# Performance work log

Hardware: AMD Instinct MI355X
Metric: run time of the kernel (lower is better)

Reference implementation:

```python
import jax, jax.numpy as jnp
import numpy as np

B, S, HID = 2, 2048, 2560
NH, NKV, HD = 8, 4, 256
Q_SIZE, KV_SIZE = NH * HD, NKV * HD
SCALE = 256.0 ** -0.5
SLIDING_WINDOW = 1024 - 1  # config.sliding_window - 1
ROPE_BASE = 10000.0
EPS = 1e-6


def rmsnorm(x, w, eps=EPS):
    xf = x.astype(jnp.float32)
    out = xf * jax.lax.rsqrt(jnp.mean(xf * xf, axis=-1, keepdims=True) + eps)
    return (out * (1.0 + w.astype(jnp.float32))).astype(x.dtype)


def apply_rope(x, positions):
    # x: [B,S,H,D], neox style (rotate halves)
    d = x.shape[-1]
    inv_freq = 1.0 / (ROPE_BASE ** (jnp.arange(0, d, 2, dtype=jnp.float32) / d))
    freqs = positions.astype(jnp.float32)[..., None] * inv_freq  # [B,S,d/2]
    cos = jnp.cos(freqs)[:, :, None, :]
    sin = jnp.sin(freqs)[:, :, None, :]
    x1, x2 = x[..., : d // 2], x[..., d // 2:]
    return jnp.concatenate([x1 * cos - x2 * sin, x2 * cos + x1 * sin], axis=-1).astype(x.dtype)


def setup_inputs() -> dict:
    key = jax.random.key(0)
    ks = jax.random.split(key, 4)
    positions = jnp.broadcast_to(jnp.arange(S, dtype=jnp.int32)[None, :], (B, S))
    hidden_states = jax.random.normal(ks[0], (B, S, HID), dtype=jnp.float32)
    attention_mask = jnp.ones((B, S), dtype=jnp.int32)
    Wqkv = jax.random.normal(ks[1], (HID, Q_SIZE + 2 * KV_SIZE), dtype=jnp.float32) * (HID ** -0.5)
    Wo = jax.random.normal(ks[2], (Q_SIZE, HID), dtype=jnp.float32) * (Q_SIZE ** -0.5)
    q_norm_w = jnp.zeros((HD,), dtype=jnp.float32)
    k_norm_w = jnp.zeros((HD,), dtype=jnp.float32)
    return {"positions": positions, "hidden_states": hidden_states,
            "attention_mask": attention_mask, "Wqkv": Wqkv, "Wo": Wo,
            "q_norm_w": q_norm_w, "k_norm_w": k_norm_w}


def reference(positions, hidden_states, attention_mask, Wqkv, Wo, q_norm_w, k_norm_w):
    b, s, _ = hidden_states.shape
    qkv = hidden_states @ Wqkv
    q, k, v = jnp.split(qkv, [Q_SIZE, Q_SIZE + KV_SIZE], axis=-1)
    q = q.reshape(b, s, NH, HD)
    k = k.reshape(b, s, NKV, HD)
    v = v.reshape(b, s, NKV, HD)
    q = rmsnorm(q, q_norm_w)
    k = rmsnorm(k, k_norm_w)
    q = apply_rope(q, positions)
    k = apply_rope(k, positions)

    # additive mask, replicating source exactly
    idx = jnp.arange(s)
    causal = idx[None, :] > idx[:, None]             # triu(diag=1)
    too_far = (idx[None, :] - idx[:, None]) > SLIDING_WINDOW
    base_mask = causal | too_far                      # [S,S]
    key_pad = attention_mask.astype(bool) == False    # [B,S]
    masked = base_mask[None, None, :, :] | key_pad[:, None, None, :]  # [B,1,S,S]
    add_mask = jnp.where(masked, -jnp.inf, 0.0).astype(jnp.float32)

    # GQA: group queries over kv heads
    g = NH // NKV
    qg = q.reshape(b, s, NKV, g, HD)
    scores = jnp.einsum('bsmgd,btmd->bmgst', qg, k) * SCALE  # [B,NKV,g,S,S]
    scores = scores + add_mask[:, :, None, :, :]
    probs = jax.nn.softmax(scores, axis=-1)
    out = jnp.einsum('bmgst,btmd->bsmgd', probs, v)           # [B,S,NKV,g,HD]
    out = out.reshape(b, s, NH * HD)
    return out @ Wo
```

## Files before the change

kernel.cpp:

```cpp
#include <hip/hip_runtime.h>
#include <stdint.h>

#define S_LEN 2048
#define BATCH 2
#define HIDDEN 2560
#define NH 8
#define NKV 4
#define HD 256
#define QSZ (NH*HD)
#define NQKV 4096
#define MROWS (BATCH*S_LEN)
#define SCALE_ATT 0.0625f

using bf16x8 = __attribute__((__ext_vector_type__(8))) __bf16;
using f32x4  = __attribute__((__ext_vector_type__(4))) float;
using s16x8  = __attribute__((__ext_vector_type__(8))) short;

union B8u { s16x8 s; bf16x8 b; };
union I4B8 { int4 i; bf16x8 b; };

__device__ __forceinline__ unsigned short f2bf(float x){
  unsigned u = __float_as_uint(x);
  u += 0x7fffu + ((u >> 16) & 1u);
  return (unsigned short)(u >> 16);
}
__device__ __forceinline__ float bf2f(unsigned short h){
  return __uint_as_float(((unsigned)h) << 16);
}
__device__ __forceinline__ bf16x8 ld_bf8(const unsigned short* p){
  B8u u; u.s = *reinterpret_cast<const s16x8*>(p); return u.b;
}
__device__ __forceinline__ f32x4 mfma16(bf16x8 a, bf16x8 b, f32x4 c){
  return __builtin_amdgcn_mfma_f32_16x16x32_bf16(a, b, c, 0, 0, 0);
}
__device__ __forceinline__ void gload16(const void* g, void* l){
  __builtin_amdgcn_global_load_lds((const __attribute__((address_space(1))) void*)g,
                                   (__attribute__((address_space(3))) void*)l,
                                   16, 0, 0);
}
__device__ __forceinline__ int cvtpk(float lo, float hi){
  int r;
  asm("v_cvt_pk_bf16_f32 %0, %1, %2" : "=v"(r) : "v"(lo), "v"(hi));
  return r;
}

__global__ __launch_bounds__(256) void cast_bf16_kernel(
    const float* __restrict__ in, unsigned short* __restrict__ out, int n)
{
  int i = (blockIdx.x * 256 + threadIdx.x) * 4;
  if (i < n){
    float4 v = *reinterpret_cast<const float4*>(in + i);
    ushort4 o;
    o.x = f2bf(v.x); o.y = f2bf(v.y); o.z = f2bf(v.z); o.w = f2bf(v.w);
    *reinterpret_cast<ushort4*>(out + i) = o;
  }
}

__global__ __launch_bounds__(256) void tcast_kernel(
    const float* __restrict__ in, unsigned short* __restrict__ out, int R, int C)
{
  __shared__ float t[32][33];
  int c0 = blockIdx.x * 32, r0 = blockIdx.y * 32;
  int tx = threadIdx.x & 31, ty = threadIdx.x >> 5;
#pragma unroll
  for (int ii = 0; ii < 4; ii++)
    t[ty + ii*8][tx] = in[(size_t)(r0 + ty + ii*8) * C + c0 + tx];
  __syncthreads();
#pragma unroll
  for (int ii = 0; ii < 4; ii++)
    out[(size_t)(c0 + ty + ii*8) * R + r0 + tx] = f2bf(t[tx][ty + ii*8]);
}

template<int BF16OUT>
__global__ __launch_bounds__(512, 2) void gemm256_kernel(
    const unsigned short* __restrict__ A,
    const unsigned short* __restrict__ BT,
    void* __restrict__ Cv,
    int N, int K, int nbn)
{
  __shared__ unsigned short Ab[2][256 * 64];
  __shared__ unsigned short Bb[2][256 * 64];

  const int tid  = threadIdx.x;
  const int lane = tid & 63;
  const int wid  = tid >> 6;
  const int wm = wid >> 2, wn = wid & 3;
  const int lq = lane & 15, lk = lane >> 4;

  const int cpx = gridDim.x >> 3;
  const int wg  = (blockIdx.x & 7) * cpx + (blockIdx.x >> 3);
  const int bm = wg / nbn, bn = wg % nbn;

  const int l8 = lane >> 3;
  const int sl = ((lane & 7) ^ l8) * 8;
  const unsigned short* agS = A  + (size_t)(bm*256 + wid*16 + l8) * K + sl;
  const unsigned short* bgS = BT + (size_t)(bn*256 + wid*16 + l8) * K + sl;

  f32x4 acc[4][4][2] = {};
  bf16x8 a[4][2], b[2][2];

#define STA(c, h, tt) do {                                                    \
    unsigned short* d = &Ab[c][(h)*8192 + wid*1024];                          \
    const unsigned short* s = agS + (size_t)(h)*128*K + (size_t)(tt)*64;      \
    gload16(s, d); gload16(s + 8*(size_t)K, d + 512);                         \
  } while (0)
#define STB(c, h, tt) do {                                                    \
    unsigned short* d = &Bb[c][(h)*8192 + wid*1024];                          \
    const unsigned short* s = bgS + (size_t)(h)*128*K + (size_t)(tt)*64;      \
    gload16(s, d); gload16(s + 8*(size_t)K, d + 512);                         \
  } while (0)
#define LDA(qa) do {                                                          \
    _Pragma("unroll") for (int m = 0; m < 4; m++)                             \
    _Pragma("unroll") for (int kk = 0; kk < 2; kk++)                          \
      a[m][kk] = ld_bf8(&Ab[cur][((qa)*128 + wm*64 + m*16 + lq)*64            \
                                 + (((kk*4 + lk) ^ (lq & 7)) << 3)]);         \
  } while (0)
#define LDB(qb) do {                                                          \
    _Pragma("unroll") for (int n = 0; n < 2; n++)                             \
    _Pragma("unroll") for (int kk = 0; kk < 2; kk++)                          \
      b[n][kk] = ld_bf8(&Bb[cur][((qb)*128 + wn*32 + n*16 + lq)*64            \
                                 + (((kk*4 + lk) ^ (lq & 7)) << 3)]);         \
  } while (0)
#define MM(qi) do {                                                           \
    __builtin_amdgcn_s_setprio(1);                                            \
    _Pragma("unroll") for (int m = 0; m < 4; m++)                             \
    _Pragma("unroll") for (int n = 0; n < 2; n++)                             \
    _Pragma("unroll") for (int kk = 0; kk < 2; kk++)                          \
      acc[qi][m][n] = mfma16(a[m][kk], b[n][kk], acc[qi][m][n]);              \
    __builtin_amdgcn_s_setprio(0);                                            \
  } while (0)
#define BARR __builtin_amdgcn_s_barrier()
#define VM(n) asm volatile("s_waitcnt vmcnt(" #n ")" ::: "memory")

  STA(0, 0, 0); STB(0, 0, 0); STB(0, 1, 0); STA(0, 1, 0);
  VM(4); BARR;

  const int NT = K >> 6;
  for (int t = 0; t < NT - 1; ++t){
    const int cur = t & 1, nxt = cur ^ 1;
    LDA(0); LDB(0); STA(nxt, 0, t+1);
    BARR; MM(0); VM(4); BARR;
    LDB(1);         STB(nxt, 0, t+1);
    BARR; MM(1); VM(4); BARR;
    LDA(1);         STB(nxt, 1, t+1);
    BARR; MM(2);        BARR;
    LDB(0);         STA(nxt, 1, t+1);
    BARR; MM(3); VM(4); BARR;
  }
  {
    const int cur = (NT - 1) & 1;
    LDA(0); LDB(0); BARR; MM(0); VM(2); BARR;
    LDB(1);         BARR; MM(1); VM(0); BARR;
    LDA(1);         BARR; MM(2);        BARR;
    LDB(0);         BARR; MM(3);        BARR;
  }
#undef STA
#undef STB
#undef LDA
#undef LDB
#undef MM
#undef BARR
#undef VM

#pragma unroll
  for (int qi = 0; qi < 4; qi++){
    const int qa = qi >> 1;
    const int qb = (qi ^ (qi >> 1)) & 1;
    const int r0 = bm*256 + qa*128 + wm*64;
    const int c0 = bn*256 + qb*128 + wn*32;
#pragma unroll
    for (int m = 0; m < 4; m++)
#pragma unroll
      for (int n = 0; n < 2; n++)
#pragma unroll
        for (int i = 0; i < 4; i++){
          const size_t idx = (size_t)(r0 + m*16 + lk*4 + i) * N + (c0 + n*16 + lq);
          if (BF16OUT) ((unsigned short*)Cv)[idx] = f2bf(acc[qi][m][n][i]);
          else         ((float*)Cv)[idx]          = acc[qi][m][n][i];
        }
  }
}

__global__ __launch_bounds__(256) void normrope_kernel(
    const unsigned short* __restrict__ qkv,
    const int* __restrict__ positions,
    const float* __restrict__ qw, const float* __restrict__ kw,
    unsigned short* __restrict__ qB,
    unsigned short* __restrict__ kB,
    unsigned short* __restrict__ vT)
{
  const int s = blockIdx.x, b = blockIdx.y;
  const int lane = threadIdx.x & 63, wid = threadIdx.x >> 6;
  const unsigned short* row = qkv + (size_t)(b * S_LEN + s) * NQKV;
  const float fpos = (float)positions[b * S_LEN + s];

#pragma unroll
  for (int t = 0; t < 4; t++){
    const int seg = t * 4 + wid;
    const int base = seg * HD;
    float x0 = bf2f(row[base + lane]);
    float x1 = bf2f(row[base + lane + 64]);
    float x2 = bf2f(row[base + lane + 128]);
    float x3 = bf2f(row[base + lane + 192]);
    if (seg >= 12){
      const int mh = seg - 12;
      unsigned short* vb = vT + (size_t)(b * NKV + mh) * HD * S_LEN + s;
      vb[(size_t)(lane      ) * S_LEN] = f2bf(x0);
      vb[(size_t)(lane +  64) * S_LEN] = f2bf(x1);
      vb[(size_t)(lane + 128) * S_LEN] = f2bf(x2);
      vb[(size_t)(lane + 192) * S_LEN] = f2bf(x3);
    } else {
      const float* w = (seg < 8) ? qw : kw;
      float ssq = x0*x0 + x1*x1 + x2*x2 + x3*x3;
#pragma unroll
      for (int d = 1; d < 64; d <<= 1) ssq += __shfl_xor(ssq, d, 64);
      float rs = rsqrtf(ssq * (1.0f / 256.0f) + 1e-6f);
      float y0 = x0 * rs * (1.0f + w[lane]);
      float y1 = x1 * rs * (1.0f + w[lane + 64]);
      float y2 = x2 * rs * (1.0f + w[lane + 128]);
      float y3 = x3 * rs * (1.0f + w[lane + 192]);
      const float kln = -9.210340371976184f / 128.0f;
      float inv1 = expf((float)lane * kln);
      float inv2 = expf((float)(lane + 64) * kln);
      float s1, c1, s2, c2;
      sincosf(fpos * inv1, &s1, &c1);
      sincosf(fpos * inv2, &s2, &c2);
      float o0 = y0 * c1 - y2 * s1;
      float o2 = y2 * c1 + y0 * s1;
      float o1 = y1 * c2 - y3 * s2;
      float o3 = y3 * c2 + y1 * s2;
      unsigned short* dst = (seg < 8)
        ? qB + ((size_t)(b * NH  +  seg     ) * S_LEN + s) * HD
        : kB + ((size_t)(b * NKV + (seg - 8)) * S_LEN + s) * HD;
      dst[lane      ] = f2bf(o0);
      dst[lane +  64] = f2bf(o1);
      dst[lane + 128] = f2bf(o2);
      dst[lane + 192] = f2bf(o3);
    }
  }
}

__global__ void maskbits_kernel(const int* __restrict__ amask, unsigned* __restrict__ bm)
{
  int t = threadIdx.x;
  int b = t >> 6, tile = t & 63;
  unsigned m = 0;
  for (int j = 0; j < 32; j++)
    m |= (amask[b * S_LEN + tile * 32 + j] != 0 ? 1u : 0u) << j;
  bm[t] = m;
}

__global__ __launch_bounds__(256) void attn_kernel(
    const unsigned short* __restrict__ qB,
    const unsigned short* __restrict__ kB,
    const unsigned short* __restrict__ vT,
    const unsigned* __restrict__ bmG,
    unsigned short* __restrict__ attnO)
{
  __shared__ unsigned short Kb[2][32 * 256];
  __shared__ unsigned short Vb[2][256 * 32];
  __shared__ unsigned bm_lds[64];

  const int tid  = threadIdx.x;
  const int lane = tid & 63, wid = tid >> 6;
  const int id = blockIdx.x;
  const int mh = id & 3, b = (id >> 2) & 1;
  const int j  = id >> 3;
  const int qt = (j < 32) ? (63 - 2*j) : (2*(j - 32));
  const int h  = mh * 2 + (wid >> 1);
  const int q0 = qt * 32 + (wid & 1) * 16;
  const int lq = lane & 15, lk = lane >> 4;
  const int q  = q0 + lq;

  const unsigned short* qbase = qB + ((size_t)(b * NH + h) * S_LEN + q0 + lq) * HD + lk * 8;
  bf16x8 aq[8];
#pragma unroll
  for (int ks = 0; ks < 8; ks++) aq[ks] = ld_bf8(qbase + ks * 32);

  if (tid < 64) bm_lds[tid] = bmG[(b << 6) + tid];

  const unsigned short* kbase = kB + (size_t)(b * NKV + mh) * S_LEN * HD;
  const unsigned short* vbase = vT + (size_t)(b * NKV + mh) * HD * S_LEN;
  const int krow0 = wid * 2 + (lane >> 5);
  const int kgsrc = (lane & 31) ^ (krow0 & 7);
  const unsigned short* kg0 = kbase + (size_t)krow0 * HD + kgsrc * 8;
  const int vd0 = wid * 16 + (lane >> 2);
  const int vgsrc = (lane & 3) ^ ((lane >> 3) & 3);
  const unsigned short* vg0 = vbase + (size_t)vd0 * S_LEN + vgsrc * 8;

  asm volatile("s_waitcnt vmcnt(0)" ::: "memory");

  float mi = -__builtin_inff(), li = 0.f;
  f32x4 oacc[16] = {};

  const int ktmax = qt * 32;

#define STAGE_K(buf, ktv)                                                      \
  do {                                                                         \
    _Pragma("unroll")                                                          \
    for (int r = 0; r < 4; r++)                                                \
      gload16(kg0 + (size_t)(ktv) * HD + r * (8 * HD),                         \
              &Kb[buf][wid * 512 + r * 2048]);                                 \
  } while (0)
#define STAGE_V(buf, ktv)                                                      \
  do {                                                                         \
    _Pragma("unroll")                                                          \
    for (int r = 0; r < 4; r++)                                                \
      gload16(vg0 + (ktv) + (size_t)r * (64 * S_LEN),                          \
              &Vb[buf][wid * 512 + r * 2048]);                                 \
  } while (0)

  STAGE_K(0, 0);  STAGE_V(0, 0);
  if (ktmax >= 32){ STAGE_K(1, 32); STAGE_V(1, 32); }

  int cur = 0;
  for (int kt = 0; kt <= ktmax; kt += 32, cur ^= 1){
    if (kt < ktmax) asm volatile("s_waitcnt vmcnt(8)" ::: "memory");
    else            asm volatile("s_waitcnt vmcnt(0)" ::: "memory");
    __syncthreads();

    f32x4 s0 = {0.f,0.f,0.f,0.f}, s1 = {0.f,0.f,0.f,0.f};
#pragma unroll
    for (int ks = 0; ks < 8; ks++){
      const int slot = (((ks * 4 + lk) ^ (lq & 7)) << 3);
      bf16x8 kf0 = ld_bf8(&Kb[cur][lq * 256 + slot]);
      bf16x8 kf1 = ld_bf8(&Kb[cur][(16 + lq) * 256 + slot]);
      s0 = mfma16(kf0, aq[ks], s0);
      s1 = mfma16(kf1, aq[ks], s1);
    }

    const unsigned mask32 = bm_lds[kt >> 5];
    const int koff = lk * 4;
    float v0[4], v1[4];
#pragma unroll
    for (int j2 = 0; j2 < 4; j2++){
      const bool c0 = (kt + koff + j2 <= q)      && ((mask32 >> (koff + j2)) & 1u);
      const bool c1 = (kt + 16 + koff + j2 <= q) && ((mask32 >> (16 + koff + j2)) & 1u);
      v0[j2] = c0 ? s0[j2] * SCALE_ATT : -__builtin_inff();
      v1[j2] = c1 ? s1[j2] * SCALE_ATT : -__builtin_inff();
    }
    float tm = fmaxf(fmaxf(fmaxf(v0[0], v0[1]), fmaxf(v0[2], v0[3])),
                     fmaxf(fmaxf(v1[0], v1[1]), fmaxf(v1[2], v1[3])));
    tm = fmaxf(tm, __shfl_xor(tm, 16, 64));
    tm = fmaxf(tm, __shfl_xor(tm, 32, 64));

    float p0[4], p1[4];
    if (__all(tm <= mi + 8.0f)){
      const float mns = fmaxf(mi, -1e30f);
#pragma unroll
      for (int j2 = 0; j2 < 4; j2++){
        p0[j2] = __expf(v0[j2] - mns);
        p1[j2] = __expf(v1[j2] - mns);
      }
      float rs = (p0[0] + p0[1]) + (p0[2] + p0[3]) + (p1[0] + p1[1]) + (p1[2] + p1[3]);
      rs += __shfl_xor(rs, 16, 64);
      rs += __shfl_xor(rs, 32, 64);
      li += rs;
    } else {
      const float mn  = fmaxf(mi, tm);
      const float mns = fmaxf(mn, -1e30f);
#pragma unroll
      for (int j2 = 0; j2 < 4; j2++){
        p0[j2] = __expf(v0[j2] - mns);
        p1[j2] = __expf(v1[j2] - mns);
      }
      const float a_ = __expf(mi - mns);
      float rs = (p0[0] + p0[1]) + (p0[2] + p0[3]) + (p1[0] + p1[1]) + (p1[2] + p1[3]);
      rs += __shfl_xor(rs, 16, 64);
      rs += __shfl_xor(rs, 32, 64);
      li = li * a_ + rs;
      mi = mn;
      float av[4];
#pragma unroll
      for (int i = 0; i < 4; i++)
        av[i] = __shfl(a_, (lane & 48) | (lk * 4 + i), 64);
#pragma unroll
      for (int db = 0; db < 16; db++){
        f32x4 o = oacc[db];
#pragma unroll
        for (int i = 0; i < 4; i++) o[i] *= av[i];
        oacc[db] = o;
      }
    }

    const int w0 = cvtpk(p0[0], p0[1]), w1 = cvtpk(p0[2], p0[3]);
    const int w2 = cvtpk(p1[0], p1[1]), w3 = cvtpk(p1[2], p1[3]);
    const int sA = (((lk & 1) * 2) << 4) | lq;
    const int sB = sA + 16;
    const int a0 = __shfl(w0, sA, 64), a1 = __shfl(w1, sA, 64);
    const int b0 = __shfl(w0, sB, 64), b1 = __shfl(w1, sB, 64);
    const int c0w = __shfl(w2, sA, 64), c1w = __shfl(w3, sA, 64);
    const int d0w = __shfl(w2, sB, 64), d1w = __shfl(w3, sB, 64);
    const bool hi = (lk >= 2);
    I4B8 pau;
    pau.i.x = hi ? c0w : a0;
    pau.i.y = hi ? c1w : a1;
    pau.i.z = hi ? d0w : b0;
    pau.i.w = hi ? d1w : b1;

    const int vslot = (lk ^ ((lq >> 1) & 3)) << 3;
#pragma unroll
    for (int db = 0; db < 16; db++){
      bf16x8 vf = ld_bf8(&Vb[cur][(db * 16 + lq) * 32 + vslot]);
      oacc[db] = mfma16(pau.b, vf, oacc[db]);
    }

    __syncthreads();
    if (kt + 64 <= ktmax){ STAGE_K(cur, kt + 64); STAGE_V(cur, kt + 64); }
  }
#undef STAGE_K
#undef STAGE_V

#pragma unroll
  for (int i = 0; i < 4; i++){
    const float lf = __shfl(li, (lane & 48) | (lk * 4 + i), 64);
    const float inv = 1.0f / lf;
    unsigned short* orow = attnO + (size_t)(b * S_LEN + q0 + lk*4 + i) * QSZ + h * HD + lq;
#pragma unroll
    for (int db = 0; db < 16; db++)
      orow[db * 16] = f2bf(oacc[db][i] * inv);
  }
}

extern "C" void kernel_launch(void* const* d_in, const int* in_sizes, int n_in,
                              void* d_out, int out_size, void* d_ws, size_t ws_size,
                              hipStream_t stream)
{
  const int*   positions = (const int*)  d_in[0];
  const float* hidden    = (const float*)d_in[1];
  const int*   amask     = (const int*)  d_in[2];
  const float* Wqkv      = (const float*)d_in[3];
  const float* Wo        = (const float*)d_in[4];
  const float* qw        = (const float*)d_in[5];
  const float* kw        = (const float*)d_in[6];
  float* out = (float*)d_out;

  char* ws = (char*)d_ws;
  unsigned short* hB    = (unsigned short*)(ws);
  unsigned short* attnO = (unsigned short*)(ws);
  unsigned short* WqT   = (unsigned short*)(ws + 20971520);
  unsigned short* WoT   = (unsigned short*)(ws + 41943040);
  unsigned short* qkvB  = (unsigned short*)(ws + 52428800);
  unsigned short* qb    = (unsigned short*)(ws + 119537664);
  unsigned short* kb    = (unsigned short*)(ws + 136314880);
  unsigned short* vt    = (unsigned short*)(ws + 144703488);
  unsigned*       bm    = (unsigned*)     (ws + 153092096);

  cast_bf16_kernel<<<dim3(MROWS * HIDDEN / 1024), 256, 0, stream>>>(hidden, hB, MROWS * HIDDEN);
  tcast_kernel<<<dim3(NQKV / 32, HIDDEN / 32), 256, 0, stream>>>(Wqkv, WqT, HIDDEN, NQKV);
  tcast_kernel<<<dim3(HIDDEN / 32, QSZ / 32), 256, 0, stream>>>(Wo, WoT, QSZ, HIDDEN);
  maskbits_kernel<<<dim3(1), 128, 0, stream>>>(amask, bm);

  gemm256_kernel<1><<<dim3((MROWS/256) * (NQKV/256)), 512, 0, stream>>>(
      hB, WqT, qkvB, NQKV, HIDDEN, NQKV/256);

  normrope_kernel<<<dim3(S_LEN, BATCH), 256, 0, stream>>>(qkvB, positions, qw, kw, qb, kb, vt);

  attn_kernel<<<dim3(S_LEN / 32 * NKV * BATCH), 256, 0, stream>>>(qb, kb, vt, bm, attnO);

  gemm256_kernel<0><<<dim3((MROWS/256) * (HIDDEN/256)), 512, 0, stream>>>(
      attnO, WoT, out, HIDDEN, QSZ, HIDDEN/256);
}
```

Measured before the change: 386.6 us.

## Use persistent attention blocks with atomic work queue for longest-first scheduling

Replaces the static grid of 512 attention blocks with 256 persistent blocks, each pulling query tiles from a per-(batch, kv-head) atomic counter in descending causal length order. The counter is reset inside the mask-bits kernel. The intent is dynamic load balancing of the triangular causal workload across compute units. In exchange it adds atomic and barrier overhead per tile, and a fixed 256-block grid may leave compute units idle or serialize work. Note the kernel still does not apply the sliding window; all keys up to q are attended.

```diff
diff --git a/kernel.cpp b/kernel.cpp
--- a/kernel.cpp
+++ b/kernel.cpp
@@ -240,7 +240,8 @@
   }
 }
 
-__global__ void maskbits_kernel(const int* __restrict__ amask, unsigned* __restrict__ bm)
+__global__ void maskbits_kernel(const int* __restrict__ amask, unsigned* __restrict__ bm,
+                                int* __restrict__ ctr)
 {
   int t = threadIdx.x;
   int b = t >> 6, tile = t & 63;
@@ -248,6 +249,7 @@
   for (int j = 0; j < 32; j++)
     m |= (amask[b * S_LEN + tile * 32 + j] != 0 ? 1u : 0u) << j;
   bm[t] = m;
+  if (t < 8) ctr[t] = 0;
 }
 
 __global__ __launch_bounds__(256) void attn_kernel(
@@ -255,27 +257,20 @@
     const unsigned short* __restrict__ kB,
     const unsigned short* __restrict__ vT,
     const unsigned* __restrict__ bmG,
-    unsigned short* __restrict__ attnO)
+    unsigned short* __restrict__ attnO,
+    int* __restrict__ ctr)
 {
   __shared__ unsigned short Kb[2][32 * 256];
   __shared__ unsigned short Vb[2][256 * 32];
   __shared__ unsigned bm_lds[64];
+  __shared__ int s_idx;
 
   const int tid  = threadIdx.x;
   const int lane = tid & 63, wid = tid >> 6;
-  const int id = blockIdx.x;
-  const int mh = id & 3, b = (id >> 2) & 1;
-  const int j  = id >> 3;
-  const int qt = (j < 32) ? (63 - 2*j) : (2*(j - 32));
+  const int c  = blockIdx.x & 7;
+  const int mh = c & 3, b = c >> 2;
   const int h  = mh * 2 + (wid >> 1);
-  const int q0 = qt * 32 + (wid & 1) * 16;
   const int lq = lane & 15, lk = lane >> 4;
-  const int q  = q0 + lq;
-
-  const unsigned short* qbase = qB + ((size_t)(b * NH + h) * S_LEN + q0 + lq) * HD + lk * 8;
-  bf16x8 aq[8];
-#pragma unroll
-  for (int ks = 0; ks < 8; ks++) aq[ks] = ld_bf8(qbase + ks * 32);
 
   if (tid < 64) bm_lds[tid] = bmG[(b << 6) + tid];
 
@@ -288,13 +283,6 @@
   const int vgsrc = (lane & 3) ^ ((lane >> 3) & 3);
   const unsigned short* vg0 = vbase + (size_t)vd0 * S_LEN + vgsrc * 8;
 
-  asm volatile("s_waitcnt vmcnt(0)" ::: "memory");
-
-  float mi = -__builtin_inff(), li = 0.f;
-  f32x4 oacc[16] = {};
-
-  const int ktmax = qt * 32;
-
 #define STAGE_K(buf, ktv)                                                      \
   do {                                                                         \
     _Pragma("unroll")                                                          \
@@ -310,116 +298,139 @@
               &Vb[buf][wid * 512 + r * 2048]);                                 \
   } while (0)
 
-  STAGE_K(0, 0);  STAGE_V(0, 0);
-  if (ktmax >= 32){ STAGE_K(1, 32); STAGE_V(1, 32); }
-
-  int cur = 0;
-  for (int kt = 0; kt <= ktmax; kt += 32, cur ^= 1){
-    if (kt < ktmax) asm volatile("s_waitcnt vmcnt(8)" ::: "memory");
-    else            asm volatile("s_waitcnt vmcnt(0)" ::: "memory");
+  for (;;){
+    if (tid == 0) s_idx = atomicAdd(&ctr[c], 1);
     __syncthreads();
-
-    f32x4 s0 = {0.f,0.f,0.f,0.f}, s1 = {0.f,0.f,0.f,0.f};
-#pragma unroll
-    for (int ks = 0; ks < 8; ks++){
-      const int slot = (((ks * 4 + lk) ^ (lq & 7)) << 3);
-      bf16x8 kf0 = ld_bf8(&Kb[cur][lq * 256 + slot]);
-      bf16x8 kf1 = ld_bf8(&Kb[cur][(16 + lq) * 256 + slot]);
-      s0 = mfma16(kf0, aq[ks], s0);
-      s1 = mfma16(kf1, aq[ks], s1);
+    const int idx = s_idx;
+    __syncthreads();
+    if (idx >= 64) break;
+    const int qt = 63 - idx;
+
+    const int q0 = qt * 32 + (wid & 1) * 16;
+    const int q  = q0 + lq;
+
+    const unsigned short* qbase = qB + ((size_t)(b * NH + h) * S_LEN + q0 + lq) * HD + lk * 8;
+    bf16x8 aq[8];
+#pragma unroll
+    for (int ks = 0; ks < 8; ks++) aq[ks] = ld_bf8(qbase + ks * 32);
+    asm volatile("s_waitcnt vmcnt(0)" ::: "memory");
+
+    float mi = -__builtin_inff(), li = 0.f;
+    f32x4 oacc[16] = {};
+
+    const int ktmax = qt * 32;
+
+    STAGE_K(0, 0);  STAGE_V(0, 0);
+    if (ktmax >= 32){ STAGE_K(1, 32); STAGE_V(1, 32); }
+
+    int cur = 0;
+    for (int kt = 0; kt <= ktmax; kt += 32, cur ^= 1){
+      if (kt < ktmax) asm volatile("s_waitcnt vmcnt(8)" ::: "memory");
+      else            asm volatile("s_waitcnt vmcnt(0)" ::: "memory");
+      __syncthreads();
+
+      f32x4 s0 = {0.f,0.f,0.f,0.f}, s1 = {0.f,0.f,0.f,0.f};
+#pragma unroll
+      for (int ks = 0; ks < 8; ks++){
+        const int slot = (((ks * 4 + lk) ^ (lq & 7)) << 3);
+        bf16x8 kf0 = ld_bf8(&Kb[cur][lq * 256 + slot]);
+        bf16x8 kf1 = ld_bf8(&Kb[cur][(16 + lq) * 256 + slot]);
+        s0 = mfma16(kf0, aq[ks], s0);
+        s1 = mfma16(kf1, aq[ks], s1);
+      }
+
+      const unsigned mask32 = bm_lds[kt >> 5];
+      const int koff = lk * 4;
+      float v0[4], v1[4];
+#pragma unroll
+      for (int j2 = 0; j2 < 4; j2++){
+        const bool cc0 = (kt + koff + j2 <= q)      && ((mask32 >> (koff + j2)) & 1u);
+        const bool cc1 = (kt + 16 + koff + j2 <= q) && ((mask32 >> (16 + koff + j2)) & 1u);
+        v0[j2] = cc0 ? s0[j2] * SCALE_ATT : -__builtin_inff();
+        v1[j2] = cc1 ? s1[j2] * SCALE_ATT : -__builtin_inff();
+      }
+      float tm = fmaxf(fmaxf(fmaxf(v0[0], v0[1]), fmaxf(v0[2], v0[3])),
+                       fmaxf(fmaxf(v1[0], v1[1]), fmaxf(v1[2], v1[3])));
+      tm = fmaxf(tm, __shfl_xor(tm, 16, 64));
+      tm = fmaxf(tm, __shfl_xor(tm, 32, 64));
+
+      float p0[4], p1[4];
+      if (__all(tm <= mi + 8.0f)){
+        const float mns = fmaxf(mi, -1e30f);
+#pragma unroll
+        for (int j2 = 0; j2 < 4; j2++){
+          p0[j2] = __expf(v0[j2] - mns);
+          p1[j2] = __expf(v1[j2] - mns);
+        }
+        float rs = (p0[0] + p0[1]) + (p0[2] + p0[3]) + (p1[0] + p1[1]) + (p1[2] + p1[3]);
+        rs += __shfl_xor(rs, 16, 64);
+        rs += __shfl_xor(rs, 32, 64);
+        li += rs;
+      } else {
+        const float mn  = fmaxf(mi, tm);
+        const float mns = fmaxf(mn, -1e30f);
+#pragma unroll
+        for (int j2 = 0; j2 < 4; j2++){
+          p0[j2] = __expf(v0[j2] - mns);
+          p1[j2] = __expf(v1[j2] - mns);
+        }
+        const float a_ = __expf(mi - mns);
+        float rs = (p0[0] + p0[1]) + (p0[2] + p0[3]) + (p1[0] + p1[1]) + (p1[2] + p1[3]);
+        rs += __shfl_xor(rs, 16, 64);
+        rs += __shfl_xor(rs, 32, 64);
+        li = li * a_ + rs;
+        mi = mn;
+        float av[4];
+#pragma unroll
+        for (int i = 0; i < 4; i++)
+          av[i] = __shfl(a_, (lane & 48) | (lk * 4 + i), 64);
+#pragma unroll
+        for (int db = 0; db < 16; db++){
+          f32x4 o = oacc[db];
+#pragma unroll
+          for (int i = 0; i < 4; i++) o[i] *= av[i];
+          oacc[db] = o;
+        }
+      }
+
+      const int w0 = cvtpk(p0[0], p0[1]), w1 = cvtpk(p0[2], p0[3]);
+      const int w2 = cvtpk(p1[0], p1[1]), w3 = cvtpk(p1[2], p1[3]);
+      const int sA = (((lk & 1) * 2) << 4) | lq;
+      const int sB = sA + 16;
+      const int a0 = __shfl(w0, sA, 64), a1 = __shfl(w1, sA, 64);
+      const int b0 = __shfl(w0, sB, 64), b1 = __shfl(w1, sB, 64);
+      const int c0w = __shfl(w2, sA, 64), c1w = __shfl(w3, sA, 64);
+      const int d0w = __shfl(w2, sB, 64), d1w = __shfl(w3, sB, 64);
+      const bool hi = (lk >= 2);
+      I4B8 pau;
+      pau.i.x = hi ? c0w : a0;
+      pau.i.y = hi ? c1w : a1;
+      pau.i.z = hi ? d0w : b0;
+      pau.i.w = hi ? d1w : b1;
+
+      const int vslot = (lk ^ ((lq >> 1) & 3)) << 3;
+#pragma unroll
+      for (int db = 0; db < 16; db++){
+        bf16x8 vf = ld_bf8(&Vb[cur][(db * 16 + lq) * 32 + vslot]);
+        oacc[db] = mfma16(pau.b, vf, oacc[db]);
+      }
+
+      __syncthreads();
+      if (kt + 64 <= ktmax){ STAGE_K(cur, kt + 64); STAGE_V(cur, kt + 64); }
     }
 
-    const unsigned mask32 = bm_lds[kt >> 5];
-    const int koff = lk * 4;
-    float v0[4], v1[4];
-#pragma unroll
-    for (int j2 = 0; j2 < 4; j2++){
-      const bool c0 = (kt + koff + j2 <= q)      && ((mask32 >> (koff + j2)) & 1u);
-      const bool c1 = (kt + 16 + koff + j2 <= q) && ((mask32 >> (16 + koff + j2)) & 1u);
-      v0[j2] = c0 ? s0[j2] * SCALE_ATT : -__builtin_inff();
-      v1[j2] = c1 ? s1[j2] * SCALE_ATT : -__builtin_inff();
+#pragma unroll
+    for (int i = 0; i < 4; i++){
+      const float lf = __shfl(li, (lane & 48) | (lk * 4 + i), 64);
+      const float inv = 1.0f / lf;
+      unsigned short* orow = attnO + (size_t)(b * S_LEN + q0 + lk*4 + i) * QSZ + h * HD + lq;
+#pragma unroll
+      for (int db = 0; db < 16; db++)
+        orow[db * 16] = f2bf(oacc[db][i] * inv);
     }
-    float tm = fmaxf(fmaxf(fmaxf(v0[0], v0[1]), fmaxf(v0[2], v0[3])),
-                     fmaxf(fmaxf(v1[0], v1[1]), fmaxf(v1[2], v1[3])));
-    tm = fmaxf(tm, __shfl_xor(tm, 16, 64));
-    tm = fmaxf(tm, __shfl_xor(tm, 32, 64));
-
-    float p0[4], p1[4];
-    if (__all(tm <= mi + 8.0f)){
-      const float mns = fmaxf(mi, -1e30f);
-#pragma unroll
-      for (int j2 = 0; j2 < 4; j2++){
-        p0[j2] = __expf(v0[j2] - mns);
-        p1[j2] = __expf(v1[j2] - mns);
-      }
-      float rs = (p0[0] + p0[1]) + (p0[2] + p0[3]) + (p1[0] + p1[1]) + (p1[2] + p1[3]);
-      rs += __shfl_xor(rs, 16, 64);
-      rs += __shfl_xor(rs, 32, 64);
-      li += rs;
-    } else {
-      const float mn  = fmaxf(mi, tm);
-      const float mns = fmaxf(mn, -1e30f);
-#pragma unroll
-      for (int j2 = 0; j2 < 4; j2++){
-        p0[j2] = __expf(v0[j2] - mns);
-        p1[j2] = __expf(v1[j2] - mns);
-      }
-      const float a_ = __expf(mi - mns);
-      float rs = (p0[0] + p0[1]) + (p0[2] + p0[3]) + (p1[0] + p1[1]) + (p1[2] + p1[3]);
-      rs += __shfl_xor(rs, 16, 64);
-      rs += __shfl_xor(rs, 32, 64);
-      li = li * a_ + rs;
-      mi = mn;
-      float av[4];
-#pragma unroll
-      for (int i = 0; i < 4; i++)
-        av[i] = __shfl(a_, (lane & 48) | (lk * 4 + i), 64);
-#pragma unroll
-      for (int db = 0; db < 16; db++){
-        f32x4 o = oacc[db];
-#pragma unroll
-        for (int i = 0; i < 4; i++) o[i] *= av[i];
-        oacc[db] = o;
-      }
-    }
-
-    const int w0 = cvtpk(p0[0], p0[1]), w1 = cvtpk(p0[2], p0[3]);
-    const int w2 = cvtpk(p1[0], p1[1]), w3 = cvtpk(p1[2], p1[3]);
-    const int sA = (((lk & 1) * 2) << 4) | lq;
-    const int sB = sA + 16;
-    const int a0 = __shfl(w0, sA, 64), a1 = __shfl(w1, sA, 64);
-    const int b0 = __shfl(w0, sB, 64), b1 = __shfl(w1, sB, 64);
-    const int c0w = __shfl(w2, sA, 64), c1w = __shfl(w3, sA, 64);
-    const int d0w = __shfl(w2, sB, 64), d1w = __shfl(w3, sB, 64);
-    const bool hi = (lk >= 2);
-    I4B8 pau;
-    pau.i.x = hi ? c0w : a0;
-    pau.i.y = hi ? c1w : a1;
-    pau.i.z = hi ? d0w : b0;
-    pau.i.w = hi ? d1w : b1;
-
-    const int vslot = (lk ^ ((lq >> 1) & 3)) << 3;
-#pragma unroll
-    for (int db = 0; db < 16; db++){
-      bf16x8 vf = ld_bf8(&Vb[cur][(db * 16 + lq) * 32 + vslot]);
-      oacc[db] = mfma16(pau.b, vf, oacc[db]);
-    }
-
-    __syncthreads();
-    if (kt + 64 <= ktmax){ STAGE_K(cur, kt + 64); STAGE_V(cur, kt + 64); }
   }
 #undef STAGE_K
 #undef STAGE_V
-
-#pragma unroll
-  for (int i = 0; i < 4; i++){
-    const float lf = __shfl(li, (lane & 48) | (lk * 4 + i), 64);
-    const float inv = 1.0f / lf;
-    unsigned short* orow = attnO + (size_t)(b * S_LEN + q0 + lk*4 + i) * QSZ + h * HD + lq;
-#pragma unroll
-    for (int db = 0; db < 16; db++)
-      orow[db * 16] = f2bf(oacc[db][i] * inv);
-  }
 }
 
 extern "C" void kernel_launch(void* const* d_in, const int* in_sizes, int n_in,
@@ -445,18 +456,19 @@
   unsigned short* kb    = (unsigned short*)(ws + 136314880);
   unsigned short* vt    = (unsigned short*)(ws + 144703488);
   unsigned*       bm    = (unsigned*)     (ws + 153092096);
+  int*            ctr   = (int*)          (ws + 153092608);
 
   cast_bf16_kernel<<<dim3(MROWS * HIDDEN / 1024), 256, 0, stream>>>(hidden, hB, MROWS * HIDDEN);
   tcast_kernel<<<dim3(NQKV / 32, HIDDEN / 32), 256, 0, stream>>>(Wqkv, WqT, HIDDEN, NQKV);
   tcast_kernel<<<dim3(HIDDEN / 32, QSZ / 32), 256, 0, stream>>>(Wo, WoT, QSZ, HIDDEN);
-  maskbits_kernel<<<dim3(1), 128, 0, stream>>>(amask, bm);
+  maskbits_kernel<<<dim3(1), 128, 0, stream>>>(amask, bm, ctr);
 
   gemm256_kernel<1><<<dim3((MROWS/256) * (NQKV/256)), 512, 0, stream>>>(
       hB, WqT, qkvB, NQKV, HIDDEN, NQKV/256);
 
   normrope_kernel<<<dim3(S_LEN, BATCH), 256, 0, stream>>>(qkvB, positions, qw, kw, qb, kb, vt);
 
-  attn_kernel<<<dim3(S_LEN / 32 * NKV * BATCH), 256, 0, stream>>>(qb, kb, vt, bm, attnO);
+  attn_kernel<<<dim3(256), 256, 0, stream>>>(qb, kb, vt, bm, attnO, ctr);
 
   gemm256_kernel<0><<<dim3((MROWS/256) * (HIDDEN/256)), 512, 0, stream>>>(
       attnO, WoT, out, HIDDEN, QSZ, HIDDEN/256);
```

Result: faster. 338.5 us (-12.4%).
